# Kernel optimization log

Hardware: AMD Instinct MI355X
Metric: run time of the kernel (lower is better)

The kernel has to match this reference:

```python
import jax, jax.numpy as jnp
import numpy as np

B, S, D, DK, DV = 8, 2048, 256, 128, 128

def setup_inputs() -> dict:
    key = jax.random.key(0)
    ks = jax.random.split(key, 9)
    return {
        "x_q": jax.random.normal(ks[0], (B, S, D), jnp.float32),
        "x_k": jax.random.normal(ks[1], (B, S, D), jnp.float32),
        "x_v": jax.random.normal(ks[2], (B, S, D), jnp.float32),
        "Wq": jax.random.normal(ks[3], (D, DK), jnp.float32) * (1.0 / np.sqrt(D)),
        "bq": jax.random.normal(ks[4], (DK,), jnp.float32) * 0.02,
        "Wk": jax.random.normal(ks[5], (D, DK), jnp.float32) * (1.0 / np.sqrt(D)),
        "bk": jax.random.normal(ks[6], (DK,), jnp.float32) * 0.02,
        "Wv": jax.random.normal(ks[7], (D, DV), jnp.float32) * (1.0 / np.sqrt(D)),
        "bv": jax.random.normal(ks[8], (DV,), jnp.float32) * 0.02,
    }

def reference(x_q, x_k, x_v, Wq, bq, Wk, bk, Wv, bv):
    # Dense projections: [B,S,D] @ [D,dk] + bias
    q = jnp.einsum("bsd,dk->bsk", x_q, Wq) + bq
    k = jnp.einsum("bsd,dk->bsk", x_k, Wk) + bk
    v = jnp.einsum("bsd,dv->bsv", x_v, Wv) + bv
    scale = 1.0 / np.sqrt(Wq.shape[1]).astype(np.float32)  # 1/sqrt(d_k)
    scores = jnp.einsum("bqk,bsk->bqs", q, k) * scale       # [B,S,S]
    attn = jax.nn.softmax(scores, axis=-1)
    return jnp.einsum("bqs,bsv->bqv", attn, v)               # [B,S,d_v]
```

## Files before the change

### kernel.cpp

```cpp
#include <hip/hip_runtime.h>
#include <stdint.h>

typedef float    f32x4  __attribute__((ext_vector_type(4)));
typedef float    f32x16 __attribute__((ext_vector_type(16)));
typedef _Float16 f16x8  __attribute__((ext_vector_type(8)));
typedef _Float16 f16x4  __attribute__((ext_vector_type(4)));

#define SPLIT 4
#define NTILES 16

__device__ __forceinline__ f32x4 mfma16(f16x8 a, f16x8 b, f32x4 c) {
    return __builtin_amdgcn_mfma_f32_16x16x32_f16(a, b, c, 0, 0, 0);
}
__device__ __forceinline__ f32x16 mfma32(f16x8 a, f16x8 b, f32x16 c) {
    return __builtin_amdgcn_mfma_f32_32x32x16_f16(a, b, c, 0, 0, 0);
}
__device__ __forceinline__ void gll16(const _Float16* g, _Float16* l) {
    __builtin_amdgcn_global_load_lds(
        (const __attribute__((address_space(1))) void*)g,
        (__attribute__((address_space(3))) void*)l, 16, 0, 0);
}
__device__ __forceinline__ void drain_vm() {
    __builtin_amdgcn_sched_barrier(0);
    asm volatile("s_waitcnt vmcnt(0)" ::: "memory");
    __builtin_amdgcn_sched_barrier(0);
}

__global__ __launch_bounds__(256) void prep_weights(
    const float* __restrict__ Wq, const float* __restrict__ Wk,
    const float* __restrict__ Wv, _Float16* __restrict__ wt) {
    __shared__ float Ls[64 * 65];
    const int bx = blockIdx.x;
    const int w  = bx >> 3, t = bx & 7;
    const int k0 = (t >> 1) * 64, n0 = (t & 1) * 64;
    const float* W = (w == 0) ? Wq : (w == 1) ? Wk : Wv;
    const int tid = threadIdx.x;
    #pragma unroll
    for (int i = 0; i < 16; i++) {
        int idx = i * 256 + tid;
        int r = idx >> 6, c = idx & 63;
        Ls[r * 65 + c] = W[(k0 + r) * 128 + n0 + c];
    }
    __syncthreads();
    #pragma unroll
    for (int i = 0; i < 16; i++) {
        int idx = i * 256 + tid;
        int r2 = idx >> 6, c2 = idx & 63;
        wt[w * 32768 + (n0 + r2) * 256 + k0 + c2] = (_Float16)Ls[c2 * 65 + r2];
    }
}

__global__ __launch_bounds__(256) void proj_kernel(
    const float* __restrict__ xq, const float* __restrict__ xk,
    const float* __restrict__ xv, const _Float16* __restrict__ wt,
    const float* __restrict__ bq, const float* __restrict__ bk,
    const float* __restrict__ bv,
    _Float16* __restrict__ qo, _Float16* __restrict__ ko,
    _Float16* __restrict__ vt)
{
    const int mode = blockIdx.y;
    const float*    X    = mode == 0 ? xq : mode == 1 ? xk : xv;
    const float*    bias = mode == 0 ? bq : mode == 1 ? bk : bv;
    const _Float16* W    = wt + mode * 32768;

    __shared__ __align__(16) _Float16 Ls[128 * 66];

    const int tid  = threadIdx.x;
    const int wave = tid >> 6, lane = tid & 63;
    const int ln   = lane & 15, qd = lane >> 4;
    const int row0 = blockIdx.x * 64 + wave * 16;

    const float*    xrow = X + (size_t)(row0 + ln) * 256 + qd * 8;
    const _Float16* wb   = W + ln * 256 + qd * 8;

    f32x4 acc[8];
    #pragma unroll
    for (int i = 0; i < 8; i++) acc[i] = (f32x4){0.f, 0.f, 0.f, 0.f};

    #pragma unroll
    for (int kk = 0; kk < 8; kk++) {
        f32x4 a0 = *(const f32x4*)(xrow + kk * 32);
        f32x4 a1 = *(const f32x4*)(xrow + kk * 32 + 4);
        f16x8 af;
        af[0] = (_Float16)a0[0]; af[1] = (_Float16)a0[1];
        af[2] = (_Float16)a0[2]; af[3] = (_Float16)a0[3];
        af[4] = (_Float16)a1[0]; af[5] = (_Float16)a1[1];
        af[6] = (_Float16)a1[2]; af[7] = (_Float16)a1[3];
        #pragma unroll
        for (int nt = 0; nt < 8; nt++) {
            f16x8 bf = *(const f16x8*)(wb + nt * 4096 + kk * 32);
            acc[nt] = mfma16(bf, af, acc[nt]);
        }
    }

    const float SC = 0.08838834764831845f * 1.4426950408889634f;
    if (mode != 2) {
        _Float16* Y = mode == 0 ? qo : ko;
        #pragma unroll
        for (int nt = 0; nt < 8; nt++) {
            const int c0 = nt * 16 + qd * 4;
            f32x4 bb = *(const f32x4*)(bias + c0);
            f16x4 st;
            #pragma unroll
            for (int r = 0; r < 4; r++) {
                float val = acc[nt][r] + bb[r];
                if (mode == 0) val *= SC;
                st[r] = (_Float16)val;
            }
            *(f16x4*)&Y[(size_t)(row0 + ln) * 128 + c0] = st;
        }
    } else {
        const int srow = wave * 16 + ln;
        #pragma unroll
        for (int nt = 0; nt < 8; nt++) {
            const int c0 = nt * 16 + qd * 4;
            f32x4 bb = *(const f32x4*)(bias + c0);
            #pragma unroll
            for (int r = 0; r < 4; r++)
                Ls[(c0 + r) * 66 + srow] = (_Float16)(acc[nt][r] + bb[r]);
        }
        __syncthreads();
        const int bb2 = row0 >> 11;
        const int s0  = (blockIdx.x * 64) & 2047;
        #pragma unroll
        for (int i = 0; i < 4; i++) {
            int g  = i * 256 + tid;
            int dv = g >> 3, off = (g & 7) * 8;
            f16x8 v8 = *(const f16x8*)&Ls[dv * 66 + off];
            *(f16x8*)(vt + ((size_t)(bb2 * 128 + dv)) * 2048 + s0 + off) = v8;
        }
    }
}

__global__ __launch_bounds__(256, 3) void attn_kernel(
    const _Float16* __restrict__ qp, const _Float16* __restrict__ kp,
    const _Float16* __restrict__ vtp, _Float16* __restrict__ opart,
    float2* __restrict__ ml)
{
    const int bid = blockIdx.x;
    const int gx  = bid & 7;
    const int q0i = (bid >> 3) & 15;
    const int gg  = bid >> 7;
    const int g   = gg * 8 + gx;
    const int b   = g >> 2;
    const int z   = g & 3;
    const int q0  = q0i * 128;

    const int tid  = threadIdx.x;
    const int wave = tid >> 6, lane = tid & 63;
    const int ln   = lane & 31, h = lane >> 5;

    __shared__ __align__(16) _Float16 smem[16896];

    int koff[8], voff[2][4];
    #pragma unroll
    for (int kb = 0; kb < 8; kb++)
        koff[kb] = ln * 128 + (((kb * 2 + h) ^ (ln & 15)) * 8);
    const int vsw = (ln >> 1) & 3;
    #pragma unroll
    for (int kb2 = 0; kb2 < 2; kb2++)
        #pragma unroll
        for (int dvb = 0; dvb < 4; dvb++)
            voff[kb2][dvb] =
                8192 + (dvb * 32 + ln) * 32 + (((kb2 * 2 + h) ^ vsw) * 8);
    int kidx[2], vidx[2], dst[2];
    #pragma unroll
    for (int j = 0; j < 2; j++) {
        int p = wave * 128 + j * 64 + lane;
        int r = p >> 4, c = p & 15;
        kidx[j] = r * 128 + ((c ^ (r & 15)) * 8);
        vidx[j] = (p >> 2) * 2048 + (((p & 3) ^ ((p >> 3) & 3)) * 8);
        dst[j]  = (wave * 128 + j * 64) * 8;
    }

    const _Float16* qbase =
        qp + (size_t)(b * 2048 + q0 + wave * 32 + ln) * 128 + h * 8;
    f16x8 qf[8];
    #pragma unroll
    for (int kb = 0; kb < 8; kb++) qf[kb] = *(const f16x8*)(qbase + kb * 16);

    f32x16 o[4];
    #pragma unroll
    for (int i = 0; i < 4; i++) o[i] = (f32x16){};
    float m_run = -1e30f, l_run = 0.f;

    const _Float16* kbase = kp + (size_t)b * 2048 * 128;
    const _Float16* vbase = vtp + (size_t)b * 128 * 2048;
    const int kt0 = z * NTILES;

    auto stage = [&](int kt, int buf) {
        const _Float16* ks = kbase + (size_t)kt * 4096;
        const _Float16* vs = vbase + kt * 32;
        _Float16* kdst = smem + buf * 4096;
        _Float16* vdst = smem + 8192 + buf * 4096;
        #pragma unroll
        for (int j = 0; j < 2; j++) {
            gll16(ks + kidx[j], kdst + dst[j]);
            gll16(vs + vidx[j], vdst + dst[j]);
        }
    };

    auto do_tile = [&](const int BUF) {
        const int KO = BUF * 4096, VO = BUF * 4096;
        f32x16 sc = (f32x16){};
        __builtin_amdgcn_s_setprio(1);
        #pragma unroll
        for (int kb = 0; kb < 8; kb++) {
            f16x8 kf = *(const f16x8*)&smem[KO + koff[kb]];
            sc = mfma32(kf, qf[kb], sc);
        }
        __builtin_amdgcn_s_setprio(0);
        float t = sc[0];
        #pragma unroll
        for (int i = 1; i < 16; i++) t = fmaxf(t, sc[i]);
        t = fmaxf(t, __shfl_xor(t, 32));
        const float mnew  = fmaxf(m_run, t);
        const float alpha = exp2f(m_run - mnew);

        f16x4 phg[4];
        float ssum = 0.f;
        #pragma unroll
        for (int gi = 0; gi < 4; gi++) {
            #pragma unroll
            for (int e = 0; e < 4; e++) {
                float p = exp2f(sc[gi * 4 + e] - mnew);
                ssum += p;
                phg[gi][e] = (_Float16)p;
            }
        }
        ssum += __shfl_xor(ssum, 32);
        l_run = l_run * alpha + ssum;
        m_run = mnew;

        if (__any(alpha < 1.0f)) {
            #pragma unroll
            for (int dvb = 0; dvb < 4; dvb++) o[dvb] *= alpha;
        }

        #pragma unroll
        for (int kb2 = 0; kb2 < 2; kb2++) {
            f16x4 own0 = phg[2 * kb2], own1 = phg[2 * kb2 + 1];
            f16x4 send = h ? own0 : own1;
            unsigned long long sv = __builtin_bit_cast(unsigned long long, send);
            unsigned long long rv = __shfl_xor(sv, 32);
            f16x4 recv = __builtin_bit_cast(f16x4, rv);
            f16x4 lo = h ? recv : own0;
            f16x4 hi = h ? own1 : recv;
            f16x8 bf = __builtin_shufflevector(lo, hi, 0, 1, 2, 3, 4, 5, 6, 7);
            __builtin_amdgcn_s_setprio(1);
            #pragma unroll
            for (int dvb = 0; dvb < 4; dvb++) {
                f16x8 vf = *(const f16x8*)&smem[VO + voff[kb2][dvb]];
                o[dvb] = mfma32(vf, bf, o[dvb]);
            }
            __builtin_amdgcn_s_setprio(0);
        }
    };

    stage(kt0, 0);
    #pragma unroll 1
    for (int ht = 0; ht < NTILES / 2; ht++) {
        drain_vm();
        __syncthreads();
        if (2 * ht + 1 < NTILES) stage(kt0 + 2 * ht + 1, 1);
        do_tile(0);
        drain_vm();
        __syncthreads();
        if (2 * ht + 2 < NTILES) stage(kt0 + 2 * ht + 2, 0);
        do_tile(1);
    }

    drain_vm();
    __syncthreads();
    _Float16* pw = smem + wave * 4224;
    #pragma unroll
    for (int dvb = 0; dvb < 4; dvb++) {
        #pragma unroll
        for (int gi = 0; gi < 4; gi++) {
            f16x4 w4;
            #pragma unroll
            for (int e = 0; e < 4; e++) w4[e] = (_Float16)o[dvb][gi * 4 + e];
            *(f16x4*)&pw[ln * 132 + dvb * 32 + gi * 8 + h * 4] = w4;
        }
    }
    const size_t prow = (size_t)(z * 8 + b) * 2048 + q0 + wave * 32;
    __builtin_amdgcn_s_waitcnt(0);
    #pragma unroll
    for (int p = 0; p < 2; p++) {
        int q = p * 16 + (lane >> 2), part = lane & 3;
        #pragma unroll
        for (int i2 = 0; i2 < 4; i2++) {
            f16x8 v8 = *(const f16x8*)&pw[q * 132 + part * 8 + i2 * 32];
            *(f16x8*)(opart + (prow + q) * 128 + part * 8 + i2 * 32) = v8;
        }
    }
    if (lane < 32) {
        float2 v; v.x = m_run; v.y = l_run;
        ml[prow + ln] = v;
    }
}

__global__ __launch_bounds__(256) void merge_kernel(
    const _Float16* __restrict__ opart, const float2* __restrict__ ml,
    float* __restrict__ out)
{
    const int t = threadIdx.x;
    const int r = t >> 4, cg = t & 15;
    const size_t row = (size_t)blockIdx.x * 16 + r;

    float M = -1e30f;
    #pragma unroll
    for (int zi = 0; zi < SPLIT; zi++)
        M = fmaxf(M, ml[(size_t)zi * 16384 + row].x);
    float L = 0.f;
    float acc[8] = {0.f, 0.f, 0.f, 0.f, 0.f, 0.f, 0.f, 0.f};
    #pragma unroll
    for (int zi = 0; zi < SPLIT; zi++) {
        float2 p = ml[(size_t)zi * 16384 + row];
        float w = exp2f(p.x - M);
        L += w * p.y;
        f16x8 v = *(const f16x8*)&opart[((size_t)zi * 16384 + row) * 128 + cg * 8];
        #pragma unroll
        for (int j = 0; j < 8; j++) acc[j] += w * (float)v[j];
    }
    const float inv = 1.0f / L;
    float* op = out + row * 128 + cg * 8;
    f32x4 lo = (f32x4){acc[0] * inv, acc[1] * inv, acc[2] * inv, acc[3] * inv};
    f32x4 hi = (f32x4){acc[4] * inv, acc[5] * inv, acc[6] * inv, acc[7] * inv};
    *(f32x4*)op = lo;
    *(f32x4*)(op + 4) = hi;
}

extern "C" void kernel_launch(void* const* d_in, const int* in_sizes, int n_in,
                              void* d_out, int out_size, void* d_ws, size_t ws_size,
                              hipStream_t stream) {
    const float* xq = (const float*)d_in[0];
    const float* xk = (const float*)d_in[1];
    const float* xv = (const float*)d_in[2];
    const float* Wq = (const float*)d_in[3];
    const float* bq = (const float*)d_in[4];
    const float* Wk = (const float*)d_in[5];
    const float* bk = (const float*)d_in[6];
    const float* Wv = (const float*)d_in[7];
    const float* bv = (const float*)d_in[8];
    float* out = (float*)d_out;

    char* ws = (char*)d_ws;
    _Float16* wt    = (_Float16*)ws;
    _Float16* qo    = (_Float16*)(ws + 196608);
    _Float16* ko    = (_Float16*)(ws + 196608 + 4194304);
    _Float16* vt    = (_Float16*)(ws + 196608 + 2 * 4194304);
    float2*   ml    = (float2*)  (ws + 196608 + 3 * 4194304);
    _Float16* opart = (_Float16*)(ws + 196608 + 3 * 4194304 + 1048576);

    hipLaunchKernelGGL(prep_weights, dim3(24), dim3(256), 0, stream,
                       Wq, Wk, Wv, wt);
    hipLaunchKernelGGL(proj_kernel, dim3(256, 3), dim3(256), 0, stream,
                       xq, xk, xv, wt, bq, bk, bv, qo, ko, vt);
    hipLaunchKernelGGL(attn_kernel, dim3(16 * 8 * SPLIT), dim3(256), 0, stream,
                       qo, ko, vt, opart, ml);
    hipLaunchKernelGGL(merge_kernel, dim3(1024), dim3(256), 0, stream,
                       opart, ml, out);
}
```

Measured before the change: 163.6 us.

## Process 64-key phases per barrier with doubled LDS tiles

The attention loop now stages 64 keys per step instead of 32: K and V tiles double in size, with a new V swizzle over 8 chunks and 64-wide rows. Each phase computes two 32-key score blocks and does one online-softmax rescale and one max/sum reduction per 64 keys. This halves the number of barriers, vmcnt drains and rescales per key. In exchange LDS use doubles, so launch bounds drop from 3 to 2 blocks per SM, which lowers occupancy and latency hiding.

```diff
diff --git a/kernel.cpp b/kernel.cpp
--- a/kernel.cpp
+++ b/kernel.cpp
@@ -7,7 +7,7 @@
 typedef _Float16 f16x4  __attribute__((ext_vector_type(4)));
 
 #define SPLIT 4
-#define NTILES 16
+#define NPHASE 8
 
 __device__ __forceinline__ f32x4 mfma16(f16x8 a, f16x8 b, f32x4 c) {
     return __builtin_amdgcn_mfma_f32_16x16x32_f16(a, b, c, 0, 0, 0);
@@ -132,7 +132,7 @@
     }
 }
 
-__global__ __launch_bounds__(256, 3) void attn_kernel(
+__global__ __launch_bounds__(256, 2) void attn_kernel(
     const _Float16* __restrict__ qp, const _Float16* __restrict__ kp,
     const _Float16* __restrict__ vtp, _Float16* __restrict__ opart,
     float2* __restrict__ ml)
@@ -150,27 +150,28 @@
     const int wave = tid >> 6, lane = tid & 63;
     const int ln   = lane & 31, h = lane >> 5;
 
-    __shared__ __align__(16) _Float16 smem[16896];
-
-    int koff[8], voff[2][4];
+    __shared__ __align__(16) _Float16 smem[32768];
+
+    int koff[8];
     #pragma unroll
     for (int kb = 0; kb < 8; kb++)
         koff[kb] = ln * 128 + (((kb * 2 + h) ^ (ln & 15)) * 8);
-    const int vsw = (ln >> 1) & 3;
-    #pragma unroll
-    for (int kb2 = 0; kb2 < 2; kb2++)
-        #pragma unroll
-        for (int dvb = 0; dvb < 4; dvb++)
-            voff[kb2][dvb] =
-                8192 + (dvb * 32 + ln) * 32 + (((kb2 * 2 + h) ^ vsw) * 8);
-    int kidx[2], vidx[2], dst[2];
-    #pragma unroll
-    for (int j = 0; j < 2; j++) {
-        int p = wave * 128 + j * 64 + lane;
+    int vcol[4];
+    #pragma unroll
+    for (int i = 0; i < 4; i++)
+        vcol[i] = ((2 * i + h) ^ (ln & 7)) * 8;
+    int vrow[4];
+    #pragma unroll
+    for (int dvb = 0; dvb < 4; dvb++) vrow[dvb] = (dvb * 32 + ln) * 64;
+
+    int kidx[4], vidx[4], dst[4];
+    #pragma unroll
+    for (int j = 0; j < 4; j++) {
+        int p = wave * 256 + j * 64 + lane;
         int r = p >> 4, c = p & 15;
         kidx[j] = r * 128 + ((c ^ (r & 15)) * 8);
-        vidx[j] = (p >> 2) * 2048 + (((p & 3) ^ ((p >> 3) & 3)) * 8);
-        dst[j]  = (wave * 128 + j * 64) * 8;
+        vidx[j] = (p >> 3) * 2048 + (((p & 7) ^ ((p >> 3) & 7)) * 8);
+        dst[j]  = (wave * 256 + j * 64) * 8;
     }
 
     const _Float16* qbase =
@@ -186,46 +187,53 @@
 
     const _Float16* kbase = kp + (size_t)b * 2048 * 128;
     const _Float16* vbase = vtp + (size_t)b * 128 * 2048;
-    const int kt0 = z * NTILES;
-
-    auto stage = [&](int kt, int buf) {
-        const _Float16* ks = kbase + (size_t)kt * 4096;
-        const _Float16* vs = vbase + kt * 32;
-        _Float16* kdst = smem + buf * 4096;
-        _Float16* vdst = smem + 8192 + buf * 4096;
-        #pragma unroll
-        for (int j = 0; j < 2; j++) {
+    const int key0 = z * 512;
+
+    auto stage = [&](int ph, int buf) {
+        const _Float16* ks = kbase + (size_t)(key0 + ph * 64) * 128;
+        const _Float16* vs = vbase + (key0 + ph * 64);
+        _Float16* kdst = smem + buf * 8192;
+        _Float16* vdst = smem + 16384 + buf * 8192;
+        #pragma unroll
+        for (int j = 0; j < 4; j++) {
             gll16(ks + kidx[j], kdst + dst[j]);
             gll16(vs + vidx[j], vdst + dst[j]);
         }
     };
 
-    auto do_tile = [&](const int BUF) {
-        const int KO = BUF * 4096, VO = BUF * 4096;
-        f32x16 sc = (f32x16){};
+    auto do_phase = [&](const int BUF) {
+        const int KO = BUF * 8192, VO = 16384 + BUF * 8192;
+        f32x16 sa = (f32x16){}, sb = (f32x16){};
         __builtin_amdgcn_s_setprio(1);
         #pragma unroll
         for (int kb = 0; kb < 8; kb++) {
             f16x8 kf = *(const f16x8*)&smem[KO + koff[kb]];
-            sc = mfma32(kf, qf[kb], sc);
+            sa = mfma32(kf, qf[kb], sa);
+        }
+        #pragma unroll
+        for (int kb = 0; kb < 8; kb++) {
+            f16x8 kf = *(const f16x8*)&smem[KO + 4096 + koff[kb]];
+            sb = mfma32(kf, qf[kb], sb);
         }
         __builtin_amdgcn_s_setprio(0);
-        float t = sc[0];
-        #pragma unroll
-        for (int i = 1; i < 16; i++) t = fmaxf(t, sc[i]);
+        float t = fmaxf(sa[0], sb[0]);
+        #pragma unroll
+        for (int i = 1; i < 16; i++) t = fmaxf(t, fmaxf(sa[i], sb[i]));
         t = fmaxf(t, __shfl_xor(t, 32));
         const float mnew  = fmaxf(m_run, t);
         const float alpha = exp2f(m_run - mnew);
 
-        f16x4 phg[4];
+        f16x4 pa[4], pb[4];
         float ssum = 0.f;
         #pragma unroll
         for (int gi = 0; gi < 4; gi++) {
             #pragma unroll
             for (int e = 0; e < 4; e++) {
-                float p = exp2f(sc[gi * 4 + e] - mnew);
-                ssum += p;
-                phg[gi][e] = (_Float16)p;
+                float p0 = exp2f(sa[gi * 4 + e] - mnew);
+                float p1 = exp2f(sb[gi * 4 + e] - mnew);
+                ssum += p0 + p1;
+                pa[gi][e] = (_Float16)p0;
+                pb[gi][e] = (_Float16)p1;
             }
         }
         ssum += __shfl_xor(ssum, 32);
@@ -238,36 +246,43 @@
         }
 
         #pragma unroll
-        for (int kb2 = 0; kb2 < 2; kb2++) {
-            f16x4 own0 = phg[2 * kb2], own1 = phg[2 * kb2 + 1];
-            f16x4 send = h ? own0 : own1;
-            unsigned long long sv = __builtin_bit_cast(unsigned long long, send);
-            unsigned long long rv = __shfl_xor(sv, 32);
-            f16x4 recv = __builtin_bit_cast(f16x4, rv);
-            f16x4 lo = h ? recv : own0;
-            f16x4 hi = h ? own1 : recv;
-            f16x8 bf = __builtin_shufflevector(lo, hi, 0, 1, 2, 3, 4, 5, 6, 7);
-            __builtin_amdgcn_s_setprio(1);
-            #pragma unroll
-            for (int dvb = 0; dvb < 4; dvb++) {
-                f16x8 vf = *(const f16x8*)&smem[VO + voff[kb2][dvb]];
-                o[dvb] = mfma32(vf, bf, o[dvb]);
+        for (int T = 0; T < 2; T++) {
+            #pragma unroll
+            for (int kb2 = 0; kb2 < 2; kb2++) {
+                f16x4 own0 = T ? pb[2 * kb2] : pa[2 * kb2];
+                f16x4 own1 = T ? pb[2 * kb2 + 1] : pa[2 * kb2 + 1];
+                f16x4 send = h ? own0 : own1;
+                unsigned long long sv =
+                    __builtin_bit_cast(unsigned long long, send);
+                unsigned long long rv = __shfl_xor(sv, 32);
+                f16x4 recv = __builtin_bit_cast(f16x4, rv);
+                f16x4 lo = h ? recv : own0;
+                f16x4 hi = h ? own1 : recv;
+                f16x8 bf =
+                    __builtin_shufflevector(lo, hi, 0, 1, 2, 3, 4, 5, 6, 7);
+                const int vc = vcol[T * 2 + kb2];
+                __builtin_amdgcn_s_setprio(1);
+                #pragma unroll
+                for (int dvb = 0; dvb < 4; dvb++) {
+                    f16x8 vf = *(const f16x8*)&smem[VO + vrow[dvb] + vc];
+                    o[dvb] = mfma32(vf, bf, o[dvb]);
+                }
+                __builtin_amdgcn_s_setprio(0);
             }
-            __builtin_amdgcn_s_setprio(0);
         }
     };
 
-    stage(kt0, 0);
+    stage(0, 0);
     #pragma unroll 1
-    for (int ht = 0; ht < NTILES / 2; ht++) {
+    for (int hp = 0; hp < NPHASE / 2; hp++) {
         drain_vm();
         __syncthreads();
-        if (2 * ht + 1 < NTILES) stage(kt0 + 2 * ht + 1, 1);
-        do_tile(0);
+        if (2 * hp + 1 < NPHASE) stage(2 * hp + 1, 1);
+        do_phase(0);
         drain_vm();
         __syncthreads();
-        if (2 * ht + 2 < NTILES) stage(kt0 + 2 * ht + 2, 0);
-        do_tile(1);
+        if (2 * hp + 2 < NPHASE) stage(2 * hp + 2, 0);
+        do_phase(1);
     }
 
     drain_vm();
```

After: 163.7 us. About the same (+0.1%).

## Split keys six ways with uneven chunks and lazy softmax rescaling

Applied to the files above, without the earlier changes.

Raises the key-dimension split from 4 to 6 partitions (four chunks of 11 tiles and two of 10) and remaps block indices so batch comes from the low bits. This gives more blocks to fill the GPU's compute units and shortens each block's serial loop. It also adds a threshold-based lazy rescale: the running max and output accumulators are updated only when the new tile max exceeds the old one by more than 8 in log2 units, which skips the rescale multiplies on most tiles. The extra partitions mean more partial outputs to write and merge, and the combine stage, which is not shown, must match SPLIT=6. Lazy rescaling allows fp16 probabilities up to 2^8, which risks precision loss.

```diff
diff --git a/kernel.cpp b/kernel.cpp
--- a/kernel.cpp
+++ b/kernel.cpp
@@ -6,8 +6,7 @@
 typedef _Float16 f16x8  __attribute__((ext_vector_type(8)));
 typedef _Float16 f16x4  __attribute__((ext_vector_type(4)));
 
-#define SPLIT 4
-#define NTILES 16
+#define SPLIT 6
 
 __device__ __forceinline__ f32x4 mfma16(f16x8 a, f16x8 b, f32x4 c) {
     return __builtin_amdgcn_mfma_f32_16x16x32_f16(a, b, c, 0, 0, 0);
@@ -139,12 +138,13 @@
 {
     const int bid = blockIdx.x;
     const int gx  = bid & 7;
-    const int q0i = (bid >> 3) & 15;
-    const int gg  = bid >> 7;
-    const int g   = gg * 8 + gx;
-    const int b   = g >> 2;
-    const int z   = g & 3;
+    const int rest = bid >> 3;
+    const int q0i = rest & 15;
+    const int z   = rest >> 4;
+    const int b   = gx;
     const int q0  = q0i * 128;
+    const int key0 = (z < 4) ? z * 352 : 1408 + (z - 4) * 320;
+    const int nt   = (z < 4) ? 11 : 10;
 
     const int tid  = threadIdx.x;
     const int wave = tid >> 6, lane = tid & 63;
@@ -184,9 +184,8 @@
     for (int i = 0; i < 4; i++) o[i] = (f32x16){};
     float m_run = -1e30f, l_run = 0.f;
 
-    const _Float16* kbase = kp + (size_t)b * 2048 * 128;
-    const _Float16* vbase = vtp + (size_t)b * 128 * 2048;
-    const int kt0 = z * NTILES;
+    const _Float16* kbase = kp + (size_t)b * 2048 * 128 + (size_t)key0 * 128;
+    const _Float16* vbase = vtp + (size_t)b * 128 * 2048 + key0;
 
     auto stage = [&](int kt, int buf) {
         const _Float16* ks = kbase + (size_t)kt * 4096;
@@ -210,12 +209,19 @@
             sc = mfma32(kf, qf[kb], sc);
         }
         __builtin_amdgcn_s_setprio(0);
-        float t = sc[0];
-        #pragma unroll
-        for (int i = 1; i < 16; i++) t = fmaxf(t, sc[i]);
-        t = fmaxf(t, __shfl_xor(t, 32));
-        const float mnew  = fmaxf(m_run, t);
-        const float alpha = exp2f(m_run - mnew);
+        float tm = sc[0];
+        #pragma unroll
+        for (int i = 1; i < 16; i++) tm = fmaxf(tm, sc[i]);
+        tm = fmaxf(tm, __shfl_xor(tm, 32));
+
+        if (!__all(tm - m_run <= 8.0f)) {
+            const float mnew  = fmaxf(m_run, tm);
+            const float alpha = exp2f(m_run - mnew);
+            #pragma unroll
+            for (int dvb = 0; dvb < 4; dvb++) o[dvb] *= alpha;
+            l_run *= alpha;
+            m_run = mnew;
+        }
 
         f16x4 phg[4];
         float ssum = 0.f;
@@ -223,19 +229,13 @@
         for (int gi = 0; gi < 4; gi++) {
             #pragma unroll
             for (int e = 0; e < 4; e++) {
-                float p = exp2f(sc[gi * 4 + e] - mnew);
+                float p = exp2f(sc[gi * 4 + e] - m_run);
                 ssum += p;
                 phg[gi][e] = (_Float16)p;
             }
         }
         ssum += __shfl_xor(ssum, 32);
-        l_run = l_run * alpha + ssum;
-        m_run = mnew;
-
-        if (__any(alpha < 1.0f)) {
-            #pragma unroll
-            for (int dvb = 0; dvb < 4; dvb++) o[dvb] *= alpha;
-        }
+        l_run += ssum;
 
         #pragma unroll
         for (int kb2 = 0; kb2 < 2; kb2++) {
@@ -257,17 +257,13 @@
         }
     };
 
-    stage(kt0, 0);
+    stage(0, 0);
     #pragma unroll 1
-    for (int ht = 0; ht < NTILES / 2; ht++) {
+    for (int ti = 0; ti < nt; ti++) {
         drain_vm();
         __syncthreads();
-        if (2 * ht + 1 < NTILES) stage(kt0 + 2 * ht + 1, 1);
-        do_tile(0);
-        drain_vm();
-        __syncthreads();
-        if (2 * ht + 2 < NTILES) stage(kt0 + 2 * ht + 2, 0);
-        do_tile(1);
+        if (ti + 1 < nt) stage(ti + 1, (ti + 1) & 1);
+        if (ti & 1) do_tile(1); else do_tile(0);
     }
 
     drain_vm();
```

After: 190.5 us. +16.5%, slower.

## Fuse split-K merge into attention kernel via last-block atomic counter

Applied to the files above, without the earlier changes.

Removes the separate merge kernel launch. Each attention block increments a per-(batch, q-tile) atomic counter after writing its partial output, and the last of the SPLIT blocks combines all partials and writes the final fp32 output. The counters are zeroed in prep_weights. This saves one launch and its pipeline drain in exchange for a tail where only the last block of each group does the merge serially, plus the threadfence and atomic overhead.

```diff
diff --git a/kernel.cpp b/kernel.cpp
--- a/kernel.cpp
+++ b/kernel.cpp
@@ -28,13 +28,15 @@
 
 __global__ __launch_bounds__(256) void prep_weights(
     const float* __restrict__ Wq, const float* __restrict__ Wk,
-    const float* __restrict__ Wv, _Float16* __restrict__ wt) {
+    const float* __restrict__ Wv, _Float16* __restrict__ wt,
+    int* __restrict__ cnt) {
     __shared__ float Ls[64 * 65];
     const int bx = blockIdx.x;
     const int w  = bx >> 3, t = bx & 7;
     const int k0 = (t >> 1) * 64, n0 = (t & 1) * 64;
     const float* W = (w == 0) ? Wq : (w == 1) ? Wk : Wv;
     const int tid = threadIdx.x;
+    if (bx == 0 && tid < 128) cnt[tid] = 0;
     #pragma unroll
     for (int i = 0; i < 16; i++) {
         int idx = i * 256 + tid;
@@ -135,7 +137,8 @@
 __global__ __launch_bounds__(256, 3) void attn_kernel(
     const _Float16* __restrict__ qp, const _Float16* __restrict__ kp,
     const _Float16* __restrict__ vtp, _Float16* __restrict__ opart,
-    float2* __restrict__ ml)
+    float2* __restrict__ ml, int* __restrict__ cnt,
+    float* __restrict__ out)
 {
     const int bid = blockIdx.x;
     const int gx  = bid & 7;
@@ -298,37 +301,47 @@
         float2 v; v.x = m_run; v.y = l_run;
         ml[prow + ln] = v;
     }
-}
-
-__global__ __launch_bounds__(256) void merge_kernel(
-    const _Float16* __restrict__ opart, const float2* __restrict__ ml,
-    float* __restrict__ out)
-{
-    const int t = threadIdx.x;
-    const int r = t >> 4, cg = t & 15;
-    const size_t row = (size_t)blockIdx.x * 16 + r;
-
-    float M = -1e30f;
-    #pragma unroll
-    for (int zi = 0; zi < SPLIT; zi++)
-        M = fmaxf(M, ml[(size_t)zi * 16384 + row].x);
-    float L = 0.f;
-    float acc[8] = {0.f, 0.f, 0.f, 0.f, 0.f, 0.f, 0.f, 0.f};
-    #pragma unroll
-    for (int zi = 0; zi < SPLIT; zi++) {
-        float2 p = ml[(size_t)zi * 16384 + row];
-        float w = exp2f(p.x - M);
-        L += w * p.y;
-        f16x8 v = *(const f16x8*)&opart[((size_t)zi * 16384 + row) * 128 + cg * 8];
-        #pragma unroll
-        for (int j = 0; j < 8; j++) acc[j] += w * (float)v[j];
-    }
-    const float inv = 1.0f / L;
-    float* op = out + row * 128 + cg * 8;
-    f32x4 lo = (f32x4){acc[0] * inv, acc[1] * inv, acc[2] * inv, acc[3] * inv};
-    f32x4 hi = (f32x4){acc[4] * inv, acc[5] * inv, acc[6] * inv, acc[7] * inv};
-    *(f32x4*)op = lo;
-    *(f32x4*)(op + 4) = hi;
+
+    __syncthreads();
+    int* sflag = (int*)smem;
+    if (tid == 0) {
+        __threadfence();
+        sflag[0] = atomicAdd(&cnt[b * 16 + q0i], 1);
+    }
+    __syncthreads();
+    if (sflag[0] == SPLIT - 1) {
+        __threadfence();
+        const int cg2 = tid & 15;
+        const int r0  = tid >> 4;
+        #pragma unroll 1
+        for (int rr = 0; rr < 8; rr++) {
+            const size_t row = (size_t)b * 2048 + q0 + r0 * 8 + rr;
+            float M = -1e30f;
+            #pragma unroll
+            for (int zi = 0; zi < SPLIT; zi++)
+                M = fmaxf(M, ml[(size_t)zi * 16384 + row].x);
+            float L = 0.f;
+            float acc[8] = {0.f, 0.f, 0.f, 0.f, 0.f, 0.f, 0.f, 0.f};
+            #pragma unroll
+            for (int zi = 0; zi < SPLIT; zi++) {
+                float2 p = ml[(size_t)zi * 16384 + row];
+                float w = exp2f(p.x - M);
+                L += w * p.y;
+                f16x8 v = *(const f16x8*)
+                    &opart[((size_t)zi * 16384 + row) * 128 + cg2 * 8];
+                #pragma unroll
+                for (int j = 0; j < 8; j++) acc[j] += w * (float)v[j];
+            }
+            const float inv = 1.0f / L;
+            float* op = out + row * 128 + cg2 * 8;
+            f32x4 lo = (f32x4){acc[0] * inv, acc[1] * inv,
+                               acc[2] * inv, acc[3] * inv};
+            f32x4 hi = (f32x4){acc[4] * inv, acc[5] * inv,
+                               acc[6] * inv, acc[7] * inv};
+            *(f32x4*)op = lo;
+            *(f32x4*)(op + 4) = hi;
+        }
+    }
 }
 
 extern "C" void kernel_launch(void* const* d_in, const int* in_sizes, int n_in,
@@ -352,13 +365,13 @@
     _Float16* vt    = (_Float16*)(ws + 196608 + 2 * 4194304);
     float2*   ml    = (float2*)  (ws + 196608 + 3 * 4194304);
     _Float16* opart = (_Float16*)(ws + 196608 + 3 * 4194304 + 1048576);
+    int*      cnt   = (int*)     (ws + 196608 + 3 * 4194304 + 1048576
+                                     + (size_t)SPLIT * 4194304);
 
     hipLaunchKernelGGL(prep_weights, dim3(24), dim3(256), 0, stream,
-                       Wq, Wk, Wv, wt);
+                       Wq, Wk, Wv, wt, cnt);
     hipLaunchKernelGGL(proj_kernel, dim3(256, 3), dim3(256), 0, stream,
                        xq, xk, xv, wt, bq, bk, bv, qo, ko, vt);
     hipLaunchKernelGGL(attn_kernel, dim3(16 * 8 * SPLIT), dim3(256), 0, stream,
-                       qo, ko, vt, opart, ml);
-    hipLaunchKernelGGL(merge_kernel, dim3(1024), dim3(256), 0, stream,
-                       opart, ml, out);
-}
+                       qo, ko, vt, opart, ml, cnt, out);
+}
```

Result: slower. 213.3 us (+30.4%).
